# Performance work log

Hardware: AMD Instinct MI355X
Metric: run time of the kernel (lower is better)

## Reference

```python
import jax, jax.numpy as jnp
import numpy as np

ATOM_TYPES = (1, 6, 7, 8)  # H, C, N, O
BN_EPS = 1e-3


def setup_inputs() -> dict:
    key = jax.random.key(0)
    k1, k2, k3 = jax.random.split(key, 3)
    B, N, M, d, L = 16, 2048, 64, 3, 12
    X = jax.random.normal(k1, (B, N, d), jnp.float32) * 4.0  # coords in Angstrom-ish scale
    # neighbor indices; offset trick guarantees no self-neighbor (avoids R=0)
    off = jax.random.randint(k2, (B, N, M), 1, N)
    Nbrs = ((jnp.arange(N)[None, :, None] + off) % N).astype(jnp.int32)
    Nbrs_Z = jax.random.randint(k3, (B, N, M), 0, 10).astype(jnp.int32)
    params = np.array([[rc, rs, 4.0] for rc in (4.0, 8.0) for rs in (0.0, 1.0, 2.0, 3.0, 4.0, 5.0)], np.float32)
    rc = jnp.asarray(params[:, 0].reshape(L, 1, 1, 1))
    rs = jnp.asarray(params[:, 1].reshape(L, 1, 1, 1))
    re = jnp.asarray(params[:, 2].reshape(L, 1, 1, 1))
    return {"X": X, "Nbrs": Nbrs, "Nbrs_Z": Nbrs_Z, "rc": rc, "rs": rs, "re": re}


def reference(X, Nbrs, Nbrs_Z, rc, rs, re):
    # gather neighbor coordinates: [B,N,M,d]
    nbr = jax.vmap(lambda coords, idx: coords[idx])(X, Nbrs)
    D = nbr - X[:, :, None, :]                      # displacement tensor [B,N,M,d]
    R = jnp.sqrt(jnp.sum(D * D, axis=-1))           # distance matrix  [B,N,M]
    R1 = R[None]                                    # [1,B,N,M], broadcasts vs [L,1,1,1]
    K = jnp.exp(-re * (R1 - rs) ** 2)               # gaussian        [L,B,N,M]
    FC = jnp.where(R1 <= rc, 0.5 * (jnp.cos(jnp.pi * R1 / rc) + 1.0), 0.0)
    rsf = K * FC                                    # radial symmetry fn [L,B,N,M]
    # per-atom-type masks [A,B,N,M]
    types = jnp.asarray(ATOM_TYPES, Nbrs_Z.dtype)
    conds = (Nbrs_Z[None] == types[:, None, None, None]).astype(rsf.dtype)
    # masked reduce over neighbors, concat over types (type-major) -> [A*L,B,N]
    sym = jnp.einsum('abnm,lbnm->albn', conds, rsf)
    A, L = sym.shape[0], sym.shape[1]
    layer = sym.reshape(A * L, sym.shape[2], sym.shape[3]).transpose(1, 2, 0)  # [B,N,A*L]
    # tf.nn.moments over axis 0 (biased variance) + batch_normalization (no scale/offset)
    m = jnp.mean(layer, axis=0)
    v = jnp.var(layer, axis=0)
    return (layer - m) / jnp.sqrt(v + BN_EPS)
```

## Files before the change

kernel.cpp:

```cpp
#include <hip/hip_runtime.h>

#define NB 16
#define NN 2048
#define NM 64
#define NC 48
#define LDSP 50
#define PIF 3.14159265358979323f

struct F3 { float x, y, z; };

__global__ __launch_bounds__(256) void fused_kernel(
    const float* __restrict__ X,
    const int* __restrict__ Nbrs,
    const int* __restrict__ NbrsZ,
    const float* __restrict__ rcg,
    const float* __restrict__ rsg,
    const float* __restrict__ reg,
    float* __restrict__ out)
{
  __shared__ float sBN[2 * NB * LDSP];

  const int tid = threadIdx.x;
  const int al  = tid >> 3;
  const int t   = tid & 7;
  const int b   = al & 15;
  const int nl  = al >> 4;
  const int n   = blockIdx.x * 2 + nl;
  const int row = b * NN + n;

  const int base = row * NM + t * 8;
  const int4 j40 = *(const int4*)(Nbrs  + base);
  const int4 j41 = *(const int4*)(Nbrs  + base + 4);
  const int4 z40 = *(const int4*)(NbrsZ + base);
  const int4 z41 = *(const int4*)(NbrsZ + base + 4);

  const float rc4 = rcg[0], rc8 = rcg[6];
  const float re  = reg[0];
  const float nre = -re;
  const float pio8  = PIF / rc8;
  const float sp    = rsg[1] - rsg[0];
  const float gcoef = 2.f * re * sp;
  const float rs3   = rsg[3];
  const float qu4 = __expf(nre * (rsg[4] * rsg[4] - rsg[3] * rsg[3]));
  const float qu5 = __expf(nre * (rsg[5] * rsg[5] - rsg[4] * rsg[4]));
  const float qd2 = __expf(nre * (rsg[2] * rsg[2] - rsg[3] * rsg[3]));
  const float qd1 = __expf(nre * (rsg[1] * rsg[1] - rsg[2] * rsg[2]));
  const float qd0 = __expf(nre * (rsg[0] * rsg[0] - rsg[1] * rsg[1]));

  const float* xb = X + (size_t)b * (NN * 3);
  const float xi = xb[n * 3 + 0];
  const float yi = xb[n * 3 + 1];
  const float zi = xb[n * 3 + 2];

  const int js[8] = {j40.x, j40.y, j40.z, j40.w, j41.x, j41.y, j41.z, j41.w};
  const int zs[8] = {z40.x, z40.y, z40.z, z40.w, z41.x, z41.y, z41.z, z41.w};

  float px[8], py[8], pz[8];
#pragma unroll
  for (int u = 0; u < 8; ++u) {
    const F3 p = *(const F3*)(xb + js[u] * 3);
    px[u] = p.x;
    py[u] = p.y;
    pz[u] = p.z;
  }

  float2 acc2[24];
#pragma unroll
  for (int c = 0; c < 24; ++c) acc2[c] = make_float2(0.f, 0.f);

#pragma unroll
  for (int u = 0; u < 8; ++u) {
    const float dx = px[u] - xi, dy = py[u] - yi, dz = pz[u] - zi;
    const float R = sqrtf(fmaf(dx, dx, fmaf(dy, dy, dz * dz)));
    const float Rk = fminf(R, rc8);

    const float u3 = Rk - rs3;
    const float K3 = __expf(nre * (u3 * u3));
    const float Gu = __expf(gcoef * Rk);
    const float Gd = __builtin_amdgcn_rcpf(Gu);
    const float K4 = K3 * Gu * qu4;
    const float K5 = K4 * Gu * qu5;
    const float K2 = K3 * Gd * qd2;
    const float K1 = K2 * Gd * qd1;
    const float K0 = K1 * Gd * qd0;
    const float K[6] = {K0, K1, K2, K3, K4, K5};

    const float c8  = __cosf(pio8 * R);
    const float c4  = fmaf(c8 + c8, c8, -1.f);
    const float fc8 = (R <= rc8) ? fmaf(0.5f, c8, 0.5f) : 0.f;
    const float fc4 = (R <= rc4) ? fmaf(0.5f, c4, 0.5f) : 0.f;

    const int z = zs[u];
    const float a40 = (z == 1) ? fc4 : 0.f, a80 = (z == 1) ? fc8 : 0.f;
    const float a41 = (z == 6) ? fc4 : 0.f, a81 = (z == 6) ? fc8 : 0.f;
    const float a42 = (z == 7) ? fc4 : 0.f, a82 = (z == 7) ? fc8 : 0.f;
    const float a43 = (z == 8) ? fc4 : 0.f, a83 = (z == 8) ? fc8 : 0.f;

#pragma unroll
    for (int r = 0; r < 6; ++r) {
      const float k = K[r];
      acc2[ 0 + r].x = fmaf(a40, k, acc2[ 0 + r].x);
      acc2[ 0 + r].y = fmaf(a80, k, acc2[ 0 + r].y);
      acc2[ 6 + r].x = fmaf(a41, k, acc2[ 6 + r].x);
      acc2[ 6 + r].y = fmaf(a81, k, acc2[ 6 + r].y);
      acc2[12 + r].x = fmaf(a42, k, acc2[12 + r].x);
      acc2[12 + r].y = fmaf(a82, k, acc2[12 + r].y);
      acc2[18 + r].x = fmaf(a43, k, acc2[18 + r].x);
      acc2[18 + r].y = fmaf(a83, k, acc2[18 + r].y);
    }
  }

  float acc[NC];
#pragma unroll
  for (int ty = 0; ty < 4; ++ty)
#pragma unroll
    for (int r = 0; r < 6; ++r) {
      acc[ty * 12 + r]     = acc2[ty * 6 + r].x;
      acc[ty * 12 + 6 + r] = acc2[ty * 6 + r].y;
    }

#pragma unroll
  for (int c = 0; c < NC; ++c) acc[c] += __shfl_xor(acc[c], 4, 64);
  const bool s4 = (t & 4) != 0;
#pragma unroll
  for (int j = 0; j < 24; ++j) acc[j] = s4 ? acc[24 + j] : acc[j];
#pragma unroll
  for (int j = 0; j < 24; ++j) acc[j] += __shfl_xor(acc[j], 2, 64);
  const bool s2 = (t & 2) != 0;
#pragma unroll
  for (int j = 0; j < 12; ++j) acc[j] = s2 ? acc[12 + j] : acc[j];
#pragma unroll
  for (int j = 0; j < 12; ++j) acc[j] += __shfl_xor(acc[j], 1, 64);
  const bool s1 = (t & 1) != 0;
  const int lb = (nl * NB + b) * LDSP + 6 * t;
#pragma unroll
  for (int j = 0; j < 6; ++j) sBN[lb + j] = s1 ? acc[6 + j] : acc[j];

  __syncthreads();

  if (tid < 128) {
    const int nn = tid >> 6;
    const int cc = tid & 63;
    if (cc < NC) {
      float x[NB];
      float s = 0.f;
#pragma unroll
      for (int bb = 0; bb < NB; ++bb) {
        x[bb] = sBN[(nn * NB + bb) * LDSP + cc];
        s += x[bb];
      }
      const float mean = s * (1.f / NB);
      float vs = 0.f;
#pragma unroll
      for (int bb = 0; bb < NB; ++bb) {
        const float d = x[bb] - mean;
        vs = fmaf(d, d, vs);
      }
      const float inv = rsqrtf(vs * (1.f / NB) + 1e-3f);
      const int ng = blockIdx.x * 2 + nn;
#pragma unroll
      for (int bb = 0; bb < NB; ++bb) {
        out[(size_t)bb * (NN * NC) + ng * NC + cc] = (x[bb] - mean) * inv;
      }
    }
  }
}

extern "C" void kernel_launch(void* const* d_in, const int* in_sizes, int n_in,
                              void* d_out, int out_size, void* d_ws, size_t ws_size,
                              hipStream_t stream) {
  const float* X   = (const float*)d_in[0];
  const int* Nbrs  = (const int*)d_in[1];
  const int* NbrsZ = (const int*)d_in[2];
  const float* rcg = (const float*)d_in[3];
  const float* rsg = (const float*)d_in[4];
  const float* reg = (const float*)d_in[5];

  float* out = (float*)d_out;

  fused_kernel<<<1024, 256, 0, stream>>>(X, Nbrs, NbrsZ, rcg, rsg, reg, out);
}
```

Before: 19.60 us.

## Split each atom row across 16 threads with one atom per block

Each block now handles a single atom across all 16 batches. Each row of 64 neighbors is split over 16 threads of 4 neighbors each instead of 8 threads of 8, and the grid doubles to 2048 blocks. This halves per-thread gather and exp work and raises parallelism, at the cost of an extra shuffle-reduction stage. Only 48 of 256 threads now do the batch-norm phase, so the final stores come from a smaller active set per block.

```diff
diff --git a/kernel.cpp b/kernel.cpp
--- a/kernel.cpp
+++ b/kernel.cpp
@@ -4,7 +4,7 @@
 #define NN 2048
 #define NM 64
 #define NC 48
-#define LDSP 50
+#define LDSP 49
 #define PIF 3.14159265358979323f
 
 struct F3 { float x, y, z; };
@@ -18,21 +18,17 @@
     const float* __restrict__ reg,
     float* __restrict__ out)
 {
-  __shared__ float sBN[2 * NB * LDSP];
+  __shared__ float sBN[NB * LDSP];
 
   const int tid = threadIdx.x;
-  const int al  = tid >> 3;
-  const int t   = tid & 7;
-  const int b   = al & 15;
-  const int nl  = al >> 4;
-  const int n   = blockIdx.x * 2 + nl;
+  const int b   = tid >> 4;
+  const int t   = tid & 15;
+  const int n   = blockIdx.x;
   const int row = b * NN + n;
 
-  const int base = row * NM + t * 8;
-  const int4 j40 = *(const int4*)(Nbrs  + base);
-  const int4 j41 = *(const int4*)(Nbrs  + base + 4);
-  const int4 z40 = *(const int4*)(NbrsZ + base);
-  const int4 z41 = *(const int4*)(NbrsZ + base + 4);
+  const int base = row * NM + t * 4;
+  const int4 j4 = *(const int4*)(Nbrs  + base);
+  const int4 z4 = *(const int4*)(NbrsZ + base);
 
   const float rc4 = rcg[0], rc8 = rcg[6];
   const float re  = reg[0];
@@ -52,12 +48,12 @@
   const float yi = xb[n * 3 + 1];
   const float zi = xb[n * 3 + 2];
 
-  const int js[8] = {j40.x, j40.y, j40.z, j40.w, j41.x, j41.y, j41.z, j41.w};
-  const int zs[8] = {z40.x, z40.y, z40.z, z40.w, z41.x, z41.y, z41.z, z41.w};
+  const int js[4] = {j4.x, j4.y, j4.z, j4.w};
+  const int zs[4] = {z4.x, z4.y, z4.z, z4.w};
 
-  float px[8], py[8], pz[8];
+  float px[4], py[4], pz[4];
 #pragma unroll
-  for (int u = 0; u < 8; ++u) {
+  for (int u = 0; u < 4; ++u) {
     const F3 p = *(const F3*)(xb + js[u] * 3);
     px[u] = p.x;
     py[u] = p.y;
@@ -69,7 +65,7 @@
   for (int c = 0; c < 24; ++c) acc2[c] = make_float2(0.f, 0.f);
 
 #pragma unroll
-  for (int u = 0; u < 8; ++u) {
+  for (int u = 0; u < 4; ++u) {
     const float dx = px[u] - xi, dy = py[u] - yi, dz = pz[u] - zi;
     const float R = sqrtf(fmaf(dx, dx, fmaf(dy, dy, dz * dz)));
     const float Rk = fminf(R, rc8);
@@ -120,48 +116,53 @@
     }
 
 #pragma unroll
-  for (int c = 0; c < NC; ++c) acc[c] += __shfl_xor(acc[c], 4, 64);
+  for (int c = 0; c < NC; ++c) acc[c] += __shfl_xor(acc[c], 8, 64);
+  const bool s8 = (t & 8) != 0;
+#pragma unroll
+  for (int j = 0; j < 24; ++j) acc[j] = s8 ? acc[24 + j] : acc[j];
+#pragma unroll
+  for (int j = 0; j < 24; ++j) acc[j] += __shfl_xor(acc[j], 4, 64);
   const bool s4 = (t & 4) != 0;
 #pragma unroll
-  for (int j = 0; j < 24; ++j) acc[j] = s4 ? acc[24 + j] : acc[j];
+  for (int j = 0; j < 12; ++j) acc[j] = s4 ? acc[12 + j] : acc[j];
 #pragma unroll
-  for (int j = 0; j < 24; ++j) acc[j] += __shfl_xor(acc[j], 2, 64);
+  for (int j = 0; j < 12; ++j) acc[j] += __shfl_xor(acc[j], 2, 64);
   const bool s2 = (t & 2) != 0;
 #pragma unroll
-  for (int j = 0; j < 12; ++j) acc[j] = s2 ? acc[12 + j] : acc[j];
+  for (int j = 0; j < 6; ++j) acc[j] = s2 ? acc[6 + j] : acc[j];
 #pragma unroll
-  for (int j = 0; j < 12; ++j) acc[j] += __shfl_xor(acc[j], 1, 64);
+  for (int j = 0; j < 6; ++j) acc[j] += __shfl_xor(acc[j], 1, 64);
   const bool s1 = (t & 1) != 0;
-  const int lb = (nl * NB + b) * LDSP + 6 * t;
 #pragma unroll
-  for (int j = 0; j < 6; ++j) sBN[lb + j] = s1 ? acc[6 + j] : acc[j];
+  for (int j = 0; j < 3; ++j) acc[j] = s1 ? acc[3 + j] : acc[j];
+
+  const int lb = b * LDSP + 3 * t;
+  sBN[lb + 0] = acc[0];
+  sBN[lb + 1] = acc[1];
+  sBN[lb + 2] = acc[2];
 
   __syncthreads();
 
-  if (tid < 128) {
-    const int nn = tid >> 6;
-    const int cc = tid & 63;
-    if (cc < NC) {
-      float x[NB];
-      float s = 0.f;
+  if (tid < NC) {
+    const int cc = tid;
+    float x[NB];
+    float s = 0.f;
 #pragma unroll
-      for (int bb = 0; bb < NB; ++bb) {
-        x[bb] = sBN[(nn * NB + bb) * LDSP + cc];
-        s += x[bb];
-      }
-      const float mean = s * (1.f / NB);
-      float vs = 0.f;
+    for (int bb = 0; bb < NB; ++bb) {
+      x[bb] = sBN[bb * LDSP + cc];
+      s += x[bb];
+    }
+    const float mean = s * (1.f / NB);
+    float vs = 0.f;
 #pragma unroll
-      for (int bb = 0; bb < NB; ++bb) {
-        const float d = x[bb] - mean;
-        vs = fmaf(d, d, vs);
-      }
-      const float inv = rsqrtf(vs * (1.f / NB) + 1e-3f);
-      const int ng = blockIdx.x * 2 + nn;
+    for (int bb = 0; bb < NB; ++bb) {
+      const float d = x[bb] - mean;
+      vs = fmaf(d, d, vs);
+    }
+    const float inv = rsqrtf(vs * (1.f / NB) + 1e-3f);
 #pragma unroll
-      for (int bb = 0; bb < NB; ++bb) {
-        out[(size_t)bb * (NN * NC) + ng * NC + cc] = (x[bb] - mean) * inv;
-      }
+    for (int bb = 0; bb < NB; ++bb) {
+      out[(size_t)bb * (NN * NC) + n * NC + cc] = (x[bb] - mean) * inv;
     }
   }
 }
@@ -178,5 +179,5 @@
 
   float* out = (float*)d_out;
 
-  fused_kernel<<<1024, 256, 0, stream>>>(X, Nbrs, NbrsZ, rcg, rsg, reg, out);
+  fused_kernel<<<2048, 256, 0, stream>>>(X, Nbrs, NbrsZ, rcg, rsg, reg, out);
 }
```

After: 18.37 us, median of 2. 6.2% less time.
